# Optimization experiments

Hardware: AMD Instinct MI355X
Metric: run time of the kernel (lower is better)

## Reference

```python
import jax, jax.numpy as jnp
import numpy as np

NUM_TOKENS = 16384
MODEL_DIM = 4096
MAX_EXPERTS = 128
INITIAL_EXPERTS = 64
THRESHOLD = 0.5  # rm_threshold


def setup_inputs() -> dict:
    key = jax.random.key(0)
    k1, k2 = jax.random.split(key)
    x = jax.random.normal(k1, (NUM_TOKENS, MODEL_DIM), dtype=jnp.float32)
    # Linear(model_dim, max_expert_num, bias=False).weight -> [E_max, D]
    wg_weight = jax.random.normal(k2, (MAX_EXPERTS, MODEL_DIM), dtype=jnp.float32) * (1.0 / np.sqrt(MODEL_DIM))
    # experts_mask: first `INITIAL_EXPERTS` active
    experts_mask = (jnp.arange(MAX_EXPERTS) < INITIAL_EXPERTS).astype(jnp.float32)
    return {"x": x, "wg_weight": wg_weight, "experts_mask": experts_mask}


def reference(x, wg_weight, experts_mask):
    # gate logits: [N, E_max]
    scores = jnp.einsum("nd,ed->ne", x, wg_weight)
    # mask inactive experts
    scores = jnp.where(experts_mask[None, :] == 0, jnp.float32(-1e9), scores)
    # fp32 softmax + epsilon (matches F.softmax(..., dtype=float32) + 1e-14)
    scores = jax.nn.softmax(scores.astype(jnp.float32), axis=-1) + 1e-14
    # sort descending along expert dim
    sorted_scores = -jnp.sort(-scores, axis=-1)
    cum_scores = jnp.cumsum(sorted_scores, axis=-1)
    # adaptive top-k: experts needed to accumulate THRESHOLD routing mass
    mask = (cum_scores - sorted_scores) < THRESHOLD
    top_k = mask.sum(axis=-1).astype(jnp.int32)
    active_experts = experts_mask.sum().astype(jnp.int32)
    top_k = jnp.minimum(top_k, active_experts)
    return scores.astype(x.dtype), top_k
```

## Files before the change

kernel.cpp:

```cpp
#include <hip/hip_runtime.h>
#include <hip/hip_bf16.h>
#include <stdint.h>

#define NTOK 16384
#define DDIM 4096
#define NEXP 128
#define BM 32
#define BK 64
#define BKP 72

typedef __attribute__((ext_vector_type(8))) short short8;
typedef __attribute__((ext_vector_type(4))) float f32x4;

__device__ __forceinline__ void split_bf16(float f, uint32_t& h, uint32_t& l) {
    uint32_t u = __float_as_uint(f);
    h = (u + 0x7FFFu + ((u >> 16) & 1u)) >> 16;
    float r = f - __uint_as_float(h << 16);
    uint32_t v = __float_as_uint(r);
    l = (v + 0x7FFFu + ((v >> 16) & 1u)) >> 16;
}

__device__ __forceinline__ void gld_lds16(const void* g, void* l) {
    __builtin_amdgcn_global_load_lds(
        (const __attribute__((address_space(1))) void*)g,
        (__attribute__((address_space(3))) void*)l, 16, 0, 0);
}

__global__ void prep_w(const float* __restrict__ w,
                       uint16_t* __restrict__ whi, uint16_t* __restrict__ wlo) {
    int i = (blockIdx.x * blockDim.x + threadIdx.x) * 4;
    float4 f = *(const float4*)(w + i);
    uint32_t h0, h1, h2, h3, l0, l1, l2, l3;
    split_bf16(f.x, h0, l0);
    split_bf16(f.y, h1, l1);
    split_bf16(f.z, h2, l2);
    split_bf16(f.w, h3, l3);
    *(uint2*)(whi + i) = make_uint2(h0 | (h1 << 16), h2 | (h3 << 16));
    *(uint2*)(wlo + i) = make_uint2(l0 | (l1 << 16), l2 | (l3 << 16));
}

__global__ __launch_bounds__(256, 2) void gate_fused(
    const float* __restrict__ x,
    const uint16_t* __restrict__ whi, const uint16_t* __restrict__ wlo,
    const float* __restrict__ mask,
    float* __restrict__ S, float* __restrict__ topk_out)
{
    __shared__ uint16_t sAh[BM * BKP], sAl[BM * BKP];
    __shared__ uint16_t sBh[NEXP * BK], sBl[NEXP * BK];
    __shared__ float    L[BM][NEXP];

    const int tid  = threadIdx.x;
    const int lane = tid & 63;
    const int wave = tid >> 6;
    const int m0   = blockIdx.x * BM;

    const float mk0 = mask[lane];
    const float mk1 = mask[lane + 64];

    const int am  = tid >> 3;
    const int akc = tid & 7;
    const float* xp = x + (size_t)(m0 + am) * DDIM + akc * 8;

    float4 fa = *(const float4*)(xp);
    float4 fb = *(const float4*)(xp + 4);

    f32x4 acc[2][2];
    #pragma unroll
    for (int mt = 0; mt < 2; ++mt)
        #pragma unroll
        for (int nt = 0; nt < 2; ++nt)
            acc[mt][nt] = (f32x4){0.f, 0.f, 0.f, 0.f};

    const int q = lane >> 4;
    const int c = lane & 15;

    int bn[4], bkc[4];
    #pragma unroll
    for (int j = 0; j < 4; ++j) {
        const int p = (wave * 4 + j) * 64 + lane;
        bn[j]  = p >> 3;
        bkc[j] = (p & 7) ^ (bn[j] & 7);
    }

    for (int k0 = 0; k0 < DDIM; k0 += BK) {
        uint32_t h[8], l[8];
        split_bf16(fa.x, h[0], l[0]); split_bf16(fa.y, h[1], l[1]);
        split_bf16(fa.z, h[2], l[2]); split_bf16(fa.w, h[3], l[3]);
        split_bf16(fb.x, h[4], l[4]); split_bf16(fb.y, h[5], l[5]);
        split_bf16(fb.z, h[6], l[6]); split_bf16(fb.w, h[7], l[7]);
        *(uint4*)&sAh[am * BKP + akc * 8] =
            make_uint4(h[0] | (h[1] << 16), h[2] | (h[3] << 16),
                       h[4] | (h[5] << 16), h[6] | (h[7] << 16));
        *(uint4*)&sAl[am * BKP + akc * 8] =
            make_uint4(l[0] | (l[1] << 16), l[2] | (l[3] << 16),
                       l[4] | (l[5] << 16), l[6] | (l[7] << 16));

        #pragma unroll
        for (int j = 0; j < 4; ++j) {
            const size_t go = (size_t)bn[j] * DDIM + k0 + bkc[j] * 8;
            const int lb = (wave * 4 + j) * 512;
            gld_lds16(whi + go, sBh + lb);
            gld_lds16(wlo + go, sBl + lb);
        }
        __syncthreads();

        {
            const int kn = (k0 + BK < DDIM) ? (k0 + BK) : 0;
            fa = *(const float4*)(xp + kn);
            fb = *(const float4*)(xp + kn + 4);
        }

        #pragma unroll
        for (int ks = 0; ks < 2; ++ks) {
            const int kb  = ks * 32 + q * 8;
            const int kb8 = ks * 4 + q;
            short8 ah[2], alo[2], bh[2], blo[2];
            #pragma unroll
            for (int mt = 0; mt < 2; ++mt) {
                const int ro = (mt * 16 + c) * BKP + kb;
                ah[mt]  = *(const short8*)&sAh[ro];
                alo[mt] = *(const short8*)&sAl[ro];
            }
            #pragma unroll
            for (int nt = 0; nt < 2; ++nt) {
                const int ne = wave * 32 + nt * 16 + c;
                const int ch = ne * 8 + (kb8 ^ (ne & 7));
                bh[nt]  = *(const short8*)&sBh[ch * 8];
                blo[nt] = *(const short8*)&sBl[ch * 8];
            }
            #pragma unroll
            for (int mt = 0; mt < 2; ++mt)
                #pragma unroll
                for (int nt = 0; nt < 2; ++nt) {
                    acc[mt][nt] = __builtin_amdgcn_mfma_f32_16x16x32_bf16(alo[mt], bh[nt],  acc[mt][nt], 0, 0, 0);
                    acc[mt][nt] = __builtin_amdgcn_mfma_f32_16x16x32_bf16(ah[mt],  blo[nt], acc[mt][nt], 0, 0, 0);
                    acc[mt][nt] = __builtin_amdgcn_mfma_f32_16x16x32_bf16(ah[mt],  bh[nt],  acc[mt][nt], 0, 0, 0);
                }
        }
        __syncthreads();
    }

    #pragma unroll
    for (int mt = 0; mt < 2; ++mt)
        #pragma unroll
        for (int nt = 0; nt < 2; ++nt) {
            const int e = wave * 32 + nt * 16 + c;
            #pragma unroll
            for (int r = 0; r < 4; ++r)
                L[mt * 16 + q * 4 + r][e] = acc[mt][nt][r];
        }
    __syncthreads();

    const bool a0 = (mk0 != 0.f), a1 = (mk1 != 0.f);
    const int active = __popcll(__ballot(a0)) + __popcll(__ballot(a1));

    for (int i = 0; i < 8; ++i) {
        const int lt  = wave * 8 + i;
        const int tok = m0 + lt;
        float s0 = L[lt][lane], s1 = L[lt][lane + 64];

        float mx = fmaxf(a0 ? s0 : -3.0e38f, a1 ? s1 : -3.0e38f);
        #pragma unroll
        for (int off = 32; off; off >>= 1) mx = fmaxf(mx, __shfl_xor(mx, off));

        float p0 = a0 ? __expf(s0 - mx) : 0.f;
        float p1 = a1 ? __expf(s1 - mx) : 0.f;
        float sum = p0 + p1;
        #pragma unroll
        for (int off = 32; off; off >>= 1) sum += __shfl_xor(sum, off);

        const float inv = 1.0f / sum;
        const float sc0 = p0 * inv + 1e-14f;
        const float sc1 = p1 * inv + 1e-14f;
        S[(size_t)tok * NEXP + lane]      = sc0;
        S[(size_t)tok * NEXP + lane + 64] = sc1;

        float v0 = sc0, v1 = sc1;
        float cum = 0.f;
        int k = 0;
        while (cum < 0.5f && k < NEXP) {
            float mv = fmaxf(v0, v1);
            #pragma unroll
            for (int off = 32; off; off >>= 1) mv = fmaxf(mv, __shfl_xor(mv, off));
            cum += mv;
            ++k;
            unsigned long long b = __ballot(v0 == mv || v1 == mv);
            int first = __ffsll(b) - 1;
            if (lane == first) {
                if (v0 == mv) v0 = -1.f; else v1 = -1.f;
            }
        }
        int topk = k < active ? k : active;
        if (lane == 0) topk_out[tok] = (float)topk;
    }
}

extern "C" void kernel_launch(void* const* d_in, const int* in_sizes, int n_in,
                              void* d_out, int out_size, void* d_ws, size_t ws_size,
                              hipStream_t stream) {
    (void)in_sizes; (void)n_in; (void)out_size; (void)ws_size;
    const float* x    = (const float*)d_in[0];
    const float* w    = (const float*)d_in[1];
    const float* mask = (const float*)d_in[2];

    float* S    = (float*)d_out;
    float* topk = S + (size_t)NTOK * NEXP;

    uint16_t* whi = (uint16_t*)d_ws;
    uint16_t* wlo = whi + (size_t)NEXP * DDIM;

    hipLaunchKernelGGL(prep_w, dim3((NEXP * DDIM) / (256 * 4)), dim3(256), 0, stream,
                       w, whi, wlo);
    hipLaunchKernelGGL(gate_fused, dim3(NTOK / BM), dim3(256), 0, stream,
                       x, whi, wlo, mask, S, topk);
}
```

Measured before the change: 433.4 us.

## Drop LDS staging and double-buffer operand fragments directly in registers

Removes the shared-memory staging of the split x tile and the async weight loads, along with both per-step block barriers. Each wave now loads its own MFMA fragments straight from global memory into registers. Two register sets are ping-ponged so the next K-step's loads are issued before the current step's MFMAs. In exchange, every wave reloads and re-splits the same x rows, so x traffic through the cache and the split ALU work are duplicated fourfold per block, and register pressure rises.

```diff
diff --git a/kernel.cpp b/kernel.cpp
--- a/kernel.cpp
+++ b/kernel.cpp
@@ -1,5 +1,4 @@
 #include <hip/hip_runtime.h>
-#include <hip/hip_bf16.h>
 #include <stdint.h>
 
 #define NTOK 16384
@@ -7,23 +6,34 @@
 #define NEXP 128
 #define BM 32
 #define BK 64
-#define BKP 72
 
 typedef __attribute__((ext_vector_type(8))) short short8;
 typedef __attribute__((ext_vector_type(4))) float f32x4;
 
+union V16 { uint4 u; short8 s; };
+
+__device__ __forceinline__ uint32_t bf16_rne(float f) {
+    uint32_t u = __float_as_uint(f);
+    return (u + 0x7FFFu + ((u >> 16) & 1u)) >> 16;
+}
+
 __device__ __forceinline__ void split_bf16(float f, uint32_t& h, uint32_t& l) {
-    uint32_t u = __float_as_uint(f);
-    h = (u + 0x7FFFu + ((u >> 16) & 1u)) >> 16;
+    h = bf16_rne(f);
     float r = f - __uint_as_float(h << 16);
-    uint32_t v = __float_as_uint(r);
-    l = (v + 0x7FFFu + ((v >> 16) & 1u)) >> 16;
-}
-
-__device__ __forceinline__ void gld_lds16(const void* g, void* l) {
-    __builtin_amdgcn_global_load_lds(
-        (const __attribute__((address_space(1))) void*)g,
-        (__attribute__((address_space(3))) void*)l, 16, 0, 0);
+    l = bf16_rne(r);
+}
+
+__device__ __forceinline__ void split8(float4 f0, float4 f1, short8& hi, short8& lo) {
+    float a[8] = {f0.x, f0.y, f0.z, f0.w, f1.x, f1.y, f1.z, f1.w};
+    uint32_t h[8], l[8];
+    #pragma unroll
+    for (int j = 0; j < 8; ++j) split_bf16(a[j], h[j], l[j]);
+    V16 H, L;
+    H.u = make_uint4(h[0] | (h[1] << 16), h[2] | (h[3] << 16),
+                     h[4] | (h[5] << 16), h[6] | (h[7] << 16));
+    L.u = make_uint4(l[0] | (l[1] << 16), l[2] | (l[3] << 16),
+                     l[4] | (l[5] << 16), l[6] | (l[7] << 16));
+    hi = H.s; lo = L.s;
 }
 
 __global__ void prep_w(const float* __restrict__ w,
@@ -39,30 +49,75 @@
     *(uint2*)(wlo + i) = make_uint2(l0 | (l1 << 16), l2 | (l3 << 16));
 }
 
+__device__ __forceinline__ void load_set(const float* xa0, const float* xa1,
+                                         const uint16_t* __restrict__ wh,
+                                         const uint16_t* __restrict__ wl,
+                                         size_t b0, size_t b1, int k0,
+                                         float4* a, uint4* b) {
+    #pragma unroll
+    for (int mt = 0; mt < 2; ++mt) {
+        const float* base = (mt ? xa1 : xa0) + k0;
+        #pragma unroll
+        for (int ks = 0; ks < 2; ++ks) {
+            a[mt * 4 + ks * 2 + 0] = *(const float4*)(base + ks * 32);
+            a[mt * 4 + ks * 2 + 1] = *(const float4*)(base + ks * 32 + 4);
+        }
+    }
+    #pragma unroll
+    for (int nt = 0; nt < 2; ++nt) {
+        const size_t off = (nt ? b1 : b0) + k0;
+        #pragma unroll
+        for (int ks = 0; ks < 2; ++ks) {
+            b[nt * 4 + ks * 2 + 0] = *(const uint4*)(wh + off + ks * 32);
+            b[nt * 4 + ks * 2 + 1] = *(const uint4*)(wl + off + ks * 32);
+        }
+    }
+}
+
+__device__ __forceinline__ void compute_set(const float4* a, const uint4* b,
+                                            f32x4 acc[2][2]) {
+    #pragma unroll
+    for (int ks = 0; ks < 2; ++ks) {
+        short8 ah[2], al[2];
+        #pragma unroll
+        for (int mt = 0; mt < 2; ++mt)
+            split8(a[mt * 4 + ks * 2], a[mt * 4 + ks * 2 + 1], ah[mt], al[mt]);
+        #pragma unroll
+        for (int mt = 0; mt < 2; ++mt)
+            #pragma unroll
+            for (int nt = 0; nt < 2; ++nt) {
+                V16 bh, bl;
+                bh.u = b[nt * 4 + ks * 2 + 0];
+                bl.u = b[nt * 4 + ks * 2 + 1];
+                acc[mt][nt] = __builtin_amdgcn_mfma_f32_16x16x32_bf16(al[mt], bh.s, acc[mt][nt], 0, 0, 0);
+                acc[mt][nt] = __builtin_amdgcn_mfma_f32_16x16x32_bf16(ah[mt], bl.s, acc[mt][nt], 0, 0, 0);
+                acc[mt][nt] = __builtin_amdgcn_mfma_f32_16x16x32_bf16(ah[mt], bh.s, acc[mt][nt], 0, 0, 0);
+            }
+    }
+}
+
 __global__ __launch_bounds__(256, 2) void gate_fused(
     const float* __restrict__ x,
     const uint16_t* __restrict__ whi, const uint16_t* __restrict__ wlo,
     const float* __restrict__ mask,
     float* __restrict__ S, float* __restrict__ topk_out)
 {
-    __shared__ uint16_t sAh[BM * BKP], sAl[BM * BKP];
-    __shared__ uint16_t sBh[NEXP * BK], sBl[NEXP * BK];
-    __shared__ float    L[BM][NEXP];
+    __shared__ float L[BM][NEXP];
 
     const int tid  = threadIdx.x;
     const int lane = tid & 63;
     const int wave = tid >> 6;
     const int m0   = blockIdx.x * BM;
+    const int q    = lane >> 4;
+    const int c    = lane & 15;
 
     const float mk0 = mask[lane];
     const float mk1 = mask[lane + 64];
 
-    const int am  = tid >> 3;
-    const int akc = tid & 7;
-    const float* xp = x + (size_t)(m0 + am) * DDIM + akc * 8;
-
-    float4 fa = *(const float4*)(xp);
-    float4 fb = *(const float4*)(xp + 4);
+    const float* xa0 = x + (size_t)(m0 + c) * DDIM + q * 8;
+    const float* xa1 = xa0 + (size_t)16 * DDIM;
+    const size_t b0 = (size_t)(wave * 32 + c) * DDIM + q * 8;
+    const size_t b1 = b0 + (size_t)16 * DDIM;
 
     f32x4 acc[2][2];
     #pragma unroll
@@ -71,73 +126,16 @@
         for (int nt = 0; nt < 2; ++nt)
             acc[mt][nt] = (f32x4){0.f, 0.f, 0.f, 0.f};
 
-    const int q = lane >> 4;
-    const int c = lane & 15;
-
-    int bn[4], bkc[4];
-    #pragma unroll
-    for (int j = 0; j < 4; ++j) {
-        const int p = (wave * 4 + j) * 64 + lane;
-        bn[j]  = p >> 3;
-        bkc[j] = (p & 7) ^ (bn[j] & 7);
-    }
-
-    for (int k0 = 0; k0 < DDIM; k0 += BK) {
-        uint32_t h[8], l[8];
-        split_bf16(fa.x, h[0], l[0]); split_bf16(fa.y, h[1], l[1]);
-        split_bf16(fa.z, h[2], l[2]); split_bf16(fa.w, h[3], l[3]);
-        split_bf16(fb.x, h[4], l[4]); split_bf16(fb.y, h[5], l[5]);
-        split_bf16(fb.z, h[6], l[6]); split_bf16(fb.w, h[7], l[7]);
-        *(uint4*)&sAh[am * BKP + akc * 8] =
-            make_uint4(h[0] | (h[1] << 16), h[2] | (h[3] << 16),
-                       h[4] | (h[5] << 16), h[6] | (h[7] << 16));
-        *(uint4*)&sAl[am * BKP + akc * 8] =
-            make_uint4(l[0] | (l[1] << 16), l[2] | (l[3] << 16),
-                       l[4] | (l[5] << 16), l[6] | (l[7] << 16));
-
-        #pragma unroll
-        for (int j = 0; j < 4; ++j) {
-            const size_t go = (size_t)bn[j] * DDIM + k0 + bkc[j] * 8;
-            const int lb = (wave * 4 + j) * 512;
-            gld_lds16(whi + go, sBh + lb);
-            gld_lds16(wlo + go, sBl + lb);
-        }
-        __syncthreads();
-
-        {
-            const int kn = (k0 + BK < DDIM) ? (k0 + BK) : 0;
-            fa = *(const float4*)(xp + kn);
-            fb = *(const float4*)(xp + kn + 4);
-        }
-
-        #pragma unroll
-        for (int ks = 0; ks < 2; ++ks) {
-            const int kb  = ks * 32 + q * 8;
-            const int kb8 = ks * 4 + q;
-            short8 ah[2], alo[2], bh[2], blo[2];
-            #pragma unroll
-            for (int mt = 0; mt < 2; ++mt) {
-                const int ro = (mt * 16 + c) * BKP + kb;
-                ah[mt]  = *(const short8*)&sAh[ro];
-                alo[mt] = *(const short8*)&sAl[ro];
-            }
-            #pragma unroll
-            for (int nt = 0; nt < 2; ++nt) {
-                const int ne = wave * 32 + nt * 16 + c;
-                const int ch = ne * 8 + (kb8 ^ (ne & 7));
-                bh[nt]  = *(const short8*)&sBh[ch * 8];
-                blo[nt] = *(const short8*)&sBl[ch * 8];
-            }
-            #pragma unroll
-            for (int mt = 0; mt < 2; ++mt)
-                #pragma unroll
-                for (int nt = 0; nt < 2; ++nt) {
-                    acc[mt][nt] = __builtin_amdgcn_mfma_f32_16x16x32_bf16(alo[mt], bh[nt],  acc[mt][nt], 0, 0, 0);
-                    acc[mt][nt] = __builtin_amdgcn_mfma_f32_16x16x32_bf16(ah[mt],  blo[nt], acc[mt][nt], 0, 0, 0);
-                    acc[mt][nt] = __builtin_amdgcn_mfma_f32_16x16x32_bf16(ah[mt],  bh[nt],  acc[mt][nt], 0, 0, 0);
-                }
-        }
-        __syncthreads();
+    float4 aR[8], aN[8];
+    uint4  bR[8], bN[8];
+    load_set(xa0, xa1, whi, wlo, b0, b1, 0, aR, bR);
+
+    for (int k0 = 0; k0 < DDIM; k0 += 2 * BK) {
+        load_set(xa0, xa1, whi, wlo, b0, b1, k0 + BK, aN, bN);
+        compute_set(aR, bR, acc);
+        const int k2 = (k0 + 2 * BK < DDIM) ? (k0 + 2 * BK) : 0;
+        load_set(xa0, xa1, whi, wlo, b0, b1, k2, aR, bR);
+        compute_set(aN, bN, acc);
     }
 
     #pragma unroll
@@ -184,8 +182,8 @@
             for (int off = 32; off; off >>= 1) mv = fmaxf(mv, __shfl_xor(mv, off));
             cum += mv;
             ++k;
-            unsigned long long b = __ballot(v0 == mv || v1 == mv);
-            int first = __ffsll(b) - 1;
+            unsigned long long bt = __ballot(v0 == mv || v1 == mv);
+            int first = __ffsll(bt) - 1;
             if (lane == first) {
                 if (v0 == mv) v0 = -1.f; else v1 = -1.f;
             }
```

After: 619.9 us. +43.0%, slower.

## Split gating GEMM from softmax/top-k postprocess and halve token tile

Applied to the files above, without the earlier changes.

Splits the fused kernel in two. A GEMM kernel with a 16-token tile and 4-block occupancy writes raw logits to the output. A separate postprocess kernel then runs softmax and adaptive top-k with one wave per token. The goal is to double the grid size and raise occupancy so the serial top-k loop no longer stalls the GEMM blocks. In exchange, each block reloads the full weight tile for half as many tokens, and the logits make an extra round trip through global memory.

```diff
diff --git a/kernel.cpp b/kernel.cpp
--- a/kernel.cpp
+++ b/kernel.cpp
@@ -1,23 +1,25 @@
 #include <hip/hip_runtime.h>
-#include <hip/hip_bf16.h>
 #include <stdint.h>
 
 #define NTOK 16384
 #define DDIM 4096
 #define NEXP 128
-#define BM 32
+#define BM 16
 #define BK 64
 #define BKP 72
 
 typedef __attribute__((ext_vector_type(8))) short short8;
 typedef __attribute__((ext_vector_type(4))) float f32x4;
 
+__device__ __forceinline__ uint32_t bf16_rne(float f) {
+    uint32_t u = __float_as_uint(f);
+    return (u + 0x7FFFu + ((u >> 16) & 1u)) >> 16;
+}
+
 __device__ __forceinline__ void split_bf16(float f, uint32_t& h, uint32_t& l) {
-    uint32_t u = __float_as_uint(f);
-    h = (u + 0x7FFFu + ((u >> 16) & 1u)) >> 16;
+    h = bf16_rne(f);
     float r = f - __uint_as_float(h << 16);
-    uint32_t v = __float_as_uint(r);
-    l = (v + 0x7FFFu + ((v >> 16) & 1u)) >> 16;
+    l = bf16_rne(r);
 }
 
 __device__ __forceinline__ void gld_lds16(const void* g, void* l) {
@@ -39,40 +41,30 @@
     *(uint2*)(wlo + i) = make_uint2(l0 | (l1 << 16), l2 | (l3 << 16));
 }
 
-__global__ __launch_bounds__(256, 2) void gate_fused(
+__global__ __launch_bounds__(256, 4) void gate_gemm(
     const float* __restrict__ x,
     const uint16_t* __restrict__ whi, const uint16_t* __restrict__ wlo,
-    const float* __restrict__ mask,
-    float* __restrict__ S, float* __restrict__ topk_out)
+    float* __restrict__ S)
 {
     __shared__ uint16_t sAh[BM * BKP], sAl[BM * BKP];
     __shared__ uint16_t sBh[NEXP * BK], sBl[NEXP * BK];
-    __shared__ float    L[BM][NEXP];
 
     const int tid  = threadIdx.x;
     const int lane = tid & 63;
     const int wave = tid >> 6;
     const int m0   = blockIdx.x * BM;
-
-    const float mk0 = mask[lane];
-    const float mk1 = mask[lane + 64];
-
-    const int am  = tid >> 3;
-    const int akc = tid & 7;
-    const float* xp = x + (size_t)(m0 + am) * DDIM + akc * 8;
+    const int q    = lane >> 4;
+    const int c    = lane & 15;
+
+    const int am  = tid >> 4;
+    const int akc = tid & 15;
+    const float* xp = x + (size_t)(m0 + am) * DDIM + akc * 4;
 
     float4 fa = *(const float4*)(xp);
-    float4 fb = *(const float4*)(xp + 4);
-
-    f32x4 acc[2][2];
-    #pragma unroll
-    for (int mt = 0; mt < 2; ++mt)
-        #pragma unroll
-        for (int nt = 0; nt < 2; ++nt)
-            acc[mt][nt] = (f32x4){0.f, 0.f, 0.f, 0.f};
-
-    const int q = lane >> 4;
-    const int c = lane & 15;
+
+    f32x4 acc[2];
+    acc[0] = (f32x4){0.f, 0.f, 0.f, 0.f};
+    acc[1] = (f32x4){0.f, 0.f, 0.f, 0.f};
 
     int bn[4], bkc[4];
     #pragma unroll
@@ -83,17 +75,13 @@
     }
 
     for (int k0 = 0; k0 < DDIM; k0 += BK) {
-        uint32_t h[8], l[8];
-        split_bf16(fa.x, h[0], l[0]); split_bf16(fa.y, h[1], l[1]);
-        split_bf16(fa.z, h[2], l[2]); split_bf16(fa.w, h[3], l[3]);
-        split_bf16(fb.x, h[4], l[4]); split_bf16(fb.y, h[5], l[5]);
-        split_bf16(fb.z, h[6], l[6]); split_bf16(fb.w, h[7], l[7]);
-        *(uint4*)&sAh[am * BKP + akc * 8] =
-            make_uint4(h[0] | (h[1] << 16), h[2] | (h[3] << 16),
-                       h[4] | (h[5] << 16), h[6] | (h[7] << 16));
-        *(uint4*)&sAl[am * BKP + akc * 8] =
-            make_uint4(l[0] | (l[1] << 16), l[2] | (l[3] << 16),
-                       l[4] | (l[5] << 16), l[6] | (l[7] << 16));
+        uint32_t h0, h1, h2, h3, l0, l1, l2, l3;
+        split_bf16(fa.x, h0, l0);
+        split_bf16(fa.y, h1, l1);
+        split_bf16(fa.z, h2, l2);
+        split_bf16(fa.w, h3, l3);
+        *(uint2*)&sAh[am * BKP + akc * 4] = make_uint2(h0 | (h1 << 16), h2 | (h3 << 16));
+        *(uint2*)&sAl[am * BKP + akc * 4] = make_uint2(l0 | (l1 << 16), l2 | (l3 << 16));
 
         #pragma unroll
         for (int j = 0; j < 4; ++j) {
@@ -107,92 +95,94 @@
         {
             const int kn = (k0 + BK < DDIM) ? (k0 + BK) : 0;
             fa = *(const float4*)(xp + kn);
-            fb = *(const float4*)(xp + kn + 4);
         }
 
         #pragma unroll
         for (int ks = 0; ks < 2; ++ks) {
             const int kb  = ks * 32 + q * 8;
             const int kb8 = ks * 4 + q;
-            short8 ah[2], alo[2], bh[2], blo[2];
-            #pragma unroll
-            for (int mt = 0; mt < 2; ++mt) {
-                const int ro = (mt * 16 + c) * BKP + kb;
-                ah[mt]  = *(const short8*)&sAh[ro];
-                alo[mt] = *(const short8*)&sAl[ro];
+            short8 ah, al, bh[2], bl[2];
+            {
+                const int ro = c * BKP + kb;
+                ah = *(const short8*)&sAh[ro];
+                al = *(const short8*)&sAl[ro];
             }
             #pragma unroll
             for (int nt = 0; nt < 2; ++nt) {
                 const int ne = wave * 32 + nt * 16 + c;
                 const int ch = ne * 8 + (kb8 ^ (ne & 7));
-                bh[nt]  = *(const short8*)&sBh[ch * 8];
-                blo[nt] = *(const short8*)&sBl[ch * 8];
+                bh[nt] = *(const short8*)&sBh[ch * 8];
+                bl[nt] = *(const short8*)&sBl[ch * 8];
             }
             #pragma unroll
-            for (int mt = 0; mt < 2; ++mt)
-                #pragma unroll
-                for (int nt = 0; nt < 2; ++nt) {
-                    acc[mt][nt] = __builtin_amdgcn_mfma_f32_16x16x32_bf16(alo[mt], bh[nt],  acc[mt][nt], 0, 0, 0);
-                    acc[mt][nt] = __builtin_amdgcn_mfma_f32_16x16x32_bf16(ah[mt],  blo[nt], acc[mt][nt], 0, 0, 0);
-                    acc[mt][nt] = __builtin_amdgcn_mfma_f32_16x16x32_bf16(ah[mt],  bh[nt],  acc[mt][nt], 0, 0, 0);
-                }
+            for (int nt = 0; nt < 2; ++nt) {
+                acc[nt] = __builtin_amdgcn_mfma_f32_16x16x32_bf16(al, bh[nt], acc[nt], 0, 0, 0);
+                acc[nt] = __builtin_amdgcn_mfma_f32_16x16x32_bf16(ah, bl[nt], acc[nt], 0, 0, 0);
+                acc[nt] = __builtin_amdgcn_mfma_f32_16x16x32_bf16(ah, bh[nt], acc[nt], 0, 0, 0);
+            }
         }
         __syncthreads();
     }
 
     #pragma unroll
-    for (int mt = 0; mt < 2; ++mt)
-        #pragma unroll
-        for (int nt = 0; nt < 2; ++nt) {
-            const int e = wave * 32 + nt * 16 + c;
-            #pragma unroll
-            for (int r = 0; r < 4; ++r)
-                L[mt * 16 + q * 4 + r][e] = acc[mt][nt][r];
-        }
-    __syncthreads();
-
+    for (int nt = 0; nt < 2; ++nt) {
+        const int e = wave * 32 + nt * 16 + c;
+        #pragma unroll
+        for (int r = 0; r < 4; ++r) {
+            const int tok = m0 + q * 4 + r;
+            S[(size_t)tok * NEXP + e] = acc[nt][r];
+        }
+    }
+}
+
+__global__ __launch_bounds__(256) void postproc(
+    float* __restrict__ S, const float* __restrict__ mask,
+    float* __restrict__ topk_out)
+{
+    const int lane = threadIdx.x & 63;
+    const int wave = threadIdx.x >> 6;
+    const int t = blockIdx.x * 4 + wave;
+    float* row = S + (size_t)t * NEXP;
+
+    float s0 = row[lane], s1 = row[lane + 64];
+    float mk0 = mask[lane], mk1 = mask[lane + 64];
     const bool a0 = (mk0 != 0.f), a1 = (mk1 != 0.f);
+
+    float mx = fmaxf(a0 ? s0 : -3.0e38f, a1 ? s1 : -3.0e38f);
+    #pragma unroll
+    for (int off = 32; off; off >>= 1) mx = fmaxf(mx, __shfl_xor(mx, off));
+
+    float p0 = a0 ? __expf(s0 - mx) : 0.f;
+    float p1 = a1 ? __expf(s1 - mx) : 0.f;
+    float sum = p0 + p1;
+    #pragma unroll
+    for (int off = 32; off; off >>= 1) sum += __shfl_xor(sum, off);
+
+    const float inv = 1.0f / sum;
+    const float sc0 = p0 * inv + 1e-14f;
+    const float sc1 = p1 * inv + 1e-14f;
+    row[lane]      = sc0;
+    row[lane + 64] = sc1;
+
     const int active = __popcll(__ballot(a0)) + __popcll(__ballot(a1));
 
-    for (int i = 0; i < 8; ++i) {
-        const int lt  = wave * 8 + i;
-        const int tok = m0 + lt;
-        float s0 = L[lt][lane], s1 = L[lt][lane + 64];
-
-        float mx = fmaxf(a0 ? s0 : -3.0e38f, a1 ? s1 : -3.0e38f);
-        #pragma unroll
-        for (int off = 32; off; off >>= 1) mx = fmaxf(mx, __shfl_xor(mx, off));
-
-        float p0 = a0 ? __expf(s0 - mx) : 0.f;
-        float p1 = a1 ? __expf(s1 - mx) : 0.f;
-        float sum = p0 + p1;
-        #pragma unroll
-        for (int off = 32; off; off >>= 1) sum += __shfl_xor(sum, off);
-
-        const float inv = 1.0f / sum;
-        const float sc0 = p0 * inv + 1e-14f;
-        const float sc1 = p1 * inv + 1e-14f;
-        S[(size_t)tok * NEXP + lane]      = sc0;
-        S[(size_t)tok * NEXP + lane + 64] = sc1;
-
-        float v0 = sc0, v1 = sc1;
-        float cum = 0.f;
-        int k = 0;
-        while (cum < 0.5f && k < NEXP) {
-            float mv = fmaxf(v0, v1);
-            #pragma unroll
-            for (int off = 32; off; off >>= 1) mv = fmaxf(mv, __shfl_xor(mv, off));
-            cum += mv;
-            ++k;
-            unsigned long long b = __ballot(v0 == mv || v1 == mv);
-            int first = __ffsll(b) - 1;
-            if (lane == first) {
-                if (v0 == mv) v0 = -1.f; else v1 = -1.f;
-            }
-        }
-        int topk = k < active ? k : active;
-        if (lane == 0) topk_out[tok] = (float)topk;
-    }
+    float v0 = sc0, v1 = sc1;
+    float cum = 0.f;
+    int k = 0;
+    while (cum < 0.5f && k < NEXP) {
+        float mv = fmaxf(v0, v1);
+        #pragma unroll
+        for (int off = 32; off; off >>= 1) mv = fmaxf(mv, __shfl_xor(mv, off));
+        cum += mv;
+        ++k;
+        unsigned long long b = __ballot(v0 == mv || v1 == mv);
+        int first = __ffsll(b) - 1;
+        if (lane == first) {
+            if (v0 == mv) v0 = -1.f; else v1 = -1.f;
+        }
+    }
+    int topk = k < active ? k : active;
+    if (lane == 0) topk_out[t] = (float)topk;
 }
 
 extern "C" void kernel_launch(void* const* d_in, const int* in_sizes, int n_in,
@@ -211,6 +201,8 @@
 
     hipLaunchKernelGGL(prep_w, dim3((NEXP * DDIM) / (256 * 4)), dim3(256), 0, stream,
                        w, whi, wlo);
-    hipLaunchKernelGGL(gate_fused, dim3(NTOK / BM), dim3(256), 0, stream,
-                       x, whi, wlo, mask, S, topk);
-}
+    hipLaunchKernelGGL(gate_gemm, dim3(NTOK / BM), dim3(256), 0, stream,
+                       x, whi, wlo, S);
+    hipLaunchKernelGGL(postproc, dim3(NTOK / 4), dim3(256), 0, stream,
+                       S, mask, topk);
+}
```

New measurement: 456.2 us. 1.05x slower.
